# Performance work log

Measured on AMD Instinct MI355X. Metric: run time of the kernel, lower is better.

Reference implementation:

```python
import jax, jax.numpy as jnp
import numpy as np

IGNORE_INDEX = -100
BETA = 0.1
B, T, H, V = 4, 512, 4096, 32000

def setup_inputs() -> dict:
    key = jax.random.key(0)
    ks = jax.random.split(key, 8)
    s = 1.0 / np.sqrt(H)
    return {
        "_input": jax.random.normal(ks[0], (B, T, H), jnp.float32),
        "weight": jax.random.normal(ks[1], (V, H), jnp.float32) * s,
        "bias": jax.random.normal(ks[2], (V,), jnp.float32) * 0.01,
        "target": jax.random.randint(ks[3], (B, T), 0, V, jnp.int64),
        "preference_labels": jax.random.bernoulli(ks[4], 0.5, (B,)),
        "ref_input": jax.random.normal(ks[5], (B, T, H), jnp.float32),
        "ref_weight": jax.random.normal(ks[6], (V, H), jnp.float32) * s,
        "ref_bias": jax.random.normal(ks[7], (V,), jnp.float32) * 0.01,
        "kl": jax.random.uniform(jax.random.fold_in(key, 9), (1,), jnp.float32),
    }

def _avg_log_prob(x, w, b, target):
    # logits: [B, T, V]
    logits = jnp.einsum("bth,vh->btv", x, w) + b
    lse = jax.nn.logsumexp(logits, axis=-1)            # [B, T]
    idx = jnp.clip(target, 0, None)[..., None]
    tgt_logit = jnp.take_along_axis(logits, idx, axis=-1)[..., 0]
    per_tok_logp = tgt_logit - lse                     # [B, T]
    mask = (target != IGNORE_INDEX).astype(per_tok_logp.dtype)
    denom = jnp.maximum(mask.sum(-1), 1.0)
    return (per_tok_logp * mask).sum(-1) / denom       # [B]

def reference(_input, weight, bias, target, preference_labels, ref_input, ref_weight, ref_bias, kl):
    avg_logp = _avg_log_prob(_input, weight, bias, target)
    ref_avg_logp = jax.lax.stop_gradient(_avg_log_prob(ref_input, ref_weight, ref_bias, target))
    logratios = avg_logp - ref_avg_logp                # [B]
    multiplier = jnp.where(preference_labels, 1.0, -1.0)
    losses = 1.0 - jax.nn.sigmoid(BETA * (logratios - kl[0]) * multiplier)
    return losses.sum() / target.shape[0]
```

## Files before the change

kernel.cpp:

```cpp
#include <hip/hip_runtime.h>
#include <hip/hip_bf16.h>
#include <stdint.h>

#define HD 4096
#define VD 32000
#define BT 2048
#define TT 512
#define IGNORE_IDX (-100)

#define BM 256
#define BN 256
#define BKT 64
#define KT (HD / BKT)
#define NB (VD / BN)
#define MB (BT / BM)
#define NWG2 (MB * NB * 2)

#define NCHUNK (VD / 64)

typedef __attribute__((ext_vector_type(8))) short short8;
typedef __attribute__((ext_vector_type(4))) float f32x4;

__device__ __forceinline__ uint16_t f2bf(float f) {
    uint32_t u = __float_as_uint(f);
    u += 0x7FFFu + ((u >> 16) & 1u);
    return (uint16_t)(u >> 16);
}

__device__ __forceinline__ void gload16(const void* g, void* l) {
    __builtin_amdgcn_global_load_lds(
        (const __attribute__((address_space(1))) void*)g,
        (__attribute__((address_space(3))) void*)l, 16, 0, 0);
}

__global__ void convert_x(const float* __restrict__ x0, const float* __restrict__ x1,
                          uint16_t* __restrict__ xbf) {
    const int64_t n4 = (int64_t)BT * HD / 4;
    ushort4* o0 = (ushort4*)xbf;
    ushort4* o1 = (ushort4*)(xbf + (int64_t)BT * HD);
    for (int64_t i = blockIdx.x * (int64_t)blockDim.x + threadIdx.x; i < n4;
         i += (int64_t)gridDim.x * blockDim.x) {
        float4 a = ((const float4*)x0)[i];
        float4 b = ((const float4*)x1)[i];
        ushort4 ua, ub;
        ua.x = f2bf(a.x); ua.y = f2bf(a.y); ua.z = f2bf(a.z); ua.w = f2bf(a.w);
        ub.x = f2bf(b.x); ub.y = f2bf(b.y); ub.z = f2bf(b.z); ub.w = f2bf(b.w);
        o0[i] = ua;
        o1[i] = ub;
    }
}

__global__ void convert_w(const float* __restrict__ w0, const float* __restrict__ w1,
                          uint16_t* __restrict__ wbf) {
    const int64_t n4 = (int64_t)VD * HD / 4;
    ushort4* o0 = (ushort4*)wbf;
    ushort4* o1 = (ushort4*)(wbf + (int64_t)VD * HD);
    for (int64_t i = blockIdx.x * (int64_t)blockDim.x + threadIdx.x; i < n4;
         i += (int64_t)gridDim.x * blockDim.x) {
        float4 a = ((const float4*)w0)[i];
        float4 b = ((const float4*)w1)[i];
        ushort4 ua, ub;
        ua.x = f2bf(a.x); ua.y = f2bf(a.y); ua.z = f2bf(a.z); ua.w = f2bf(a.w);
        ub.x = f2bf(b.x); ub.y = f2bf(b.y); ub.z = f2bf(b.z); ub.w = f2bf(b.w);
        o0[i] = ua;
        o1[i] = ub;
    }
}

template<int CUR>
__device__ __forceinline__ void tile_body(
    int t,
    const uint16_t* __restrict__ agp, const uint16_t* __restrict__ bgp, int wid,
    const char* pA0, const char* pA1, const char* pB0, const char* pB1,
    uint16_t* As, uint16_t* Bs, f32x4 (&acc)[8][4])
{
    const int nxt = CUR ^ 1;
    const bool more = (t + 1) < KT;
    const int ko = (t + 1) * BKT;

    __builtin_amdgcn_sched_barrier(0);
    asm volatile("s_waitcnt vmcnt(4)" ::: "memory");
    __builtin_amdgcn_sched_barrier(0);
    __builtin_amdgcn_s_barrier();
    __builtin_amdgcn_sched_barrier(0);
    if (more) {
#pragma unroll
        for (int i = 0; i < 4; ++i)
            gload16(bgp + (size_t)i * 8 * HD + ko,
                    (char*)Bs + nxt * 32768 + wid * 4096 + i * 1024);
    }
    __builtin_amdgcn_sched_barrier(0);
    if (more) { asm volatile("s_waitcnt vmcnt(4)" ::: "memory"); }
    else      { asm volatile("s_waitcnt vmcnt(0)" ::: "memory"); }
    __builtin_amdgcn_sched_barrier(0);
    __builtin_amdgcn_s_barrier();
    __builtin_amdgcn_sched_barrier(0);
    if (more) {
#pragma unroll
        for (int i = 0; i < 4; ++i)
            gload16(agp + (size_t)i * 8 * HD + ko,
                    (char*)As + nxt * 32768 + wid * 4096 + i * 1024);
    }

#pragma unroll
    for (int ks = 0; ks < 2; ++ks) {
        const char* pA = ks ? pA1 : pA0;
        const char* pB = ks ? pB1 : pB0;
        short8 af[8], bf[4];
#pragma unroll
        for (int mi = 0; mi < 8; ++mi)
            af[mi] = *(const short8*)(pA + mi * 2048 + CUR * 32768);
#pragma unroll
        for (int ni = 0; ni < 4; ++ni)
            bf[ni] = *(const short8*)(pB + ni * 2048 + CUR * 32768);
        __builtin_amdgcn_s_setprio(1);
#pragma unroll
        for (int mi = 0; mi < 8; ++mi)
#pragma unroll
            for (int ni = 0; ni < 4; ++ni)
                acc[mi][ni] = __builtin_amdgcn_mfma_f32_16x16x32_bf16(
                    af[mi], bf[ni], acc[mi][ni], 0, 0, 0);
        __builtin_amdgcn_s_setprio(0);
    }
}

__global__ __launch_bounds__(512, 2) void gemm_lse_bf(
    const uint16_t* __restrict__ xbf, const uint16_t* __restrict__ wbf,
    const float* __restrict__ b0, const float* __restrict__ b1,
    const int* __restrict__ target,
    float* __restrict__ partials, float* __restrict__ tgtlog)
{
    __shared__ uint16_t As[2 * BM * BKT];
    __shared__ uint16_t Bs[2 * BN * BKT];

    const int orig = blockIdx.x;
    const int wgid = (orig & 7) * (NWG2 / 8) + (orig >> 3);
    const int mb    = wgid & 7;
    const int rest  = wgid >> 3;
    const int nb    = rest % NB;
    const int model = rest / NB;

    const uint16_t* xb = xbf + (size_t)model * BT * HD;
    const uint16_t* wb = wbf + (size_t)model * VD * HD;
    const float* bias  = model ? b1 : b0;

    const int row0 = mb * BM;
    const int c0   = nb * BN;

    const int tid    = threadIdx.x;
    const int lane   = tid & 63;
    const int wid    = tid >> 6;
    const int wr     = wid >> 2;
    const int wc     = wid & 3;

    const int lane15 = lane & 15;
    const int kg     = lane >> 4;
    const int swz    = (lane & 7) << 4;

    const int srow8 = lane >> 3;
    const int slot  = (lane & 7) ^ srow8;
    const uint16_t* agp = xb + (size_t)(row0 + wid * 32 + srow8) * HD + slot * 8;
    const uint16_t* bgp = wb + (size_t)(c0   + wid * 32 + srow8) * HD + slot * 8;

    const int arow_b = wr * 128 + lane15;
    const int brow_b = wc * 64 + lane15;
    const char* pA0 = (const char*)As + ((arow_b * 128 + 0  + kg * 16) ^ swz);
    const char* pA1 = (const char*)As + ((arow_b * 128 + 64 + kg * 16) ^ swz);
    const char* pB0 = (const char*)Bs + ((brow_b * 128 + 0  + kg * 16) ^ swz);
    const char* pB1 = (const char*)Bs + ((brow_b * 128 + 64 + kg * 16) ^ swz);

    f32x4 acc[8][4];
#pragma unroll
    for (int i = 0; i < 8; ++i)
#pragma unroll
        for (int j = 0; j < 4; ++j) acc[i][j] = (f32x4){0.f, 0.f, 0.f, 0.f};

#pragma unroll
    for (int i = 0; i < 4; ++i)
        gload16(bgp + (size_t)i * 8 * HD, (char*)Bs + wid * 4096 + i * 1024);
#pragma unroll
    for (int i = 0; i < 4; ++i)
        gload16(agp + (size_t)i * 8 * HD, (char*)As + wid * 4096 + i * 1024);

    for (int t2 = 0; t2 < KT; t2 += 2) {
        tile_body<0>(t2,     agp, bgp, wid, pA0, pA1, pB0, pB1, As, Bs, acc);
        tile_body<1>(t2 + 1, agp, bgp, wid, pA0, pA1, pB0, pB1, As, Bs, acc);
    }

    float bv4[4];
#pragma unroll
    for (int ni = 0; ni < 4; ++ni) bv4[ni] = bias[c0 + wc * 64 + ni * 16 + lane15];

#pragma unroll
    for (int mi = 0; mi < 8; ++mi) {
        const int grow_base = row0 + wr * 128 + mi * 16 + kg * 4;
#pragma unroll
        for (int j = 0; j < 4; ++j) {
            const int grow = grow_base + j;
            float v[4];
#pragma unroll
            for (int ni = 0; ni < 4; ++ni) v[ni] = acc[mi][ni][j] + bv4[ni];
            float m = fmaxf(fmaxf(v[0], v[1]), fmaxf(v[2], v[3]));
#pragma unroll
            for (int msk = 1; msk < 16; msk <<= 1)
                m = fmaxf(m, __shfl_xor(m, msk));
            float s = __expf(v[0] - m) + __expf(v[1] - m) +
                      __expf(v[2] - m) + __expf(v[3] - m);
#pragma unroll
            for (int msk = 1; msk < 16; msk <<= 1)
                s += __shfl_xor(s, msk);
            const int tg = target[grow];
#pragma unroll
            for (int ni = 0; ni < 4; ++ni) {
                const int gcol = c0 + wc * 64 + ni * 16 + lane15;
                if (tg == gcol) tgtlog[model * BT + grow] = v[ni];
            }
            if (lane15 == 0) {
                const size_t po = ((size_t)(model * BT + grow) * NCHUNK + nb * 4 + wc) * 2;
                partials[po]     = m;
                partials[po + 1] = s;
            }
        }
    }
}

__global__ __launch_bounds__(256) void gemm_lse_f32(
    const uint16_t* __restrict__ xbf,
    const float* __restrict__ w0, const float* __restrict__ b0,
    const float* __restrict__ w1, const float* __restrict__ b1,
    const int* __restrict__ target,
    float* __restrict__ partials, float* __restrict__ tgtlog)
{
    const int orig = blockIdx.x;
    const int wgid = (orig & 7) * 1000 + (orig >> 3);
    const int mb    = wgid & 7;
    const int rest  = wgid >> 3;
    const int chunk = rest % 500;
    const int model = rest / 500;

    const float* w    = model ? w1 : w0;
    const float* bias = model ? b1 : b0;
    const uint16_t* xb = xbf + (size_t)model * BT * HD;

    const int row0 = mb * 256;
    const int c0   = chunk * 64;

    const int tid  = threadIdx.x;
    const int lane = tid & 63;
    const int wid  = tid >> 6;

    __shared__ uint16_t As_[256 * 64];
    __shared__ uint16_t Bs_[64 * 64];

    f32x4 acc[4][4];
#pragma unroll
    for (int i = 0; i < 4; ++i)
#pragma unroll
        for (int j = 0; j < 4; ++j) acc[i][j] = (f32x4){0.f, 0.f, 0.f, 0.f};

    const int srow8 = lane >> 3;
    const int slot  = (lane & 7) ^ srow8;
    const uint16_t* agsrc = xb + (size_t)(row0 + wid * 64 + srow8) * HD + slot * 8;
    char* aldst = (char*)As_ + wid * 8192;

    const int ss   = tid & 7;
    const int srow = tid >> 3;
    const int swz_w = (srow & 7) << 4;
    const float* bptr = w + (size_t)(c0 + srow) * HD + ss * 8;

    const int lane15 = lane & 15;
    const int kg     = lane >> 4;
    const int swz_r  = (lane & 7) << 4;

    for (int kt = 0; kt < 64; ++kt) {
        const int kofs = kt * 64;
#pragma unroll
        for (int c = 0; c < 8; ++c)
            gload16(agsrc + (size_t)c * 8 * HD + kofs, aldst + c * 1024);
        {
            float4 bv[2][2];
#pragma unroll
            for (int r = 0; r < 2; ++r) {
                const float* p = bptr + (size_t)r * 32 * HD + kofs;
                bv[r][0] = *(const float4*)(p);
                bv[r][1] = *(const float4*)(p + 4);
            }
#pragma unroll
            for (int r = 0; r < 2; ++r) {
                const int row_l = srow + r * 32;
                float fv[8] = {bv[r][0].x, bv[r][0].y, bv[r][0].z, bv[r][0].w,
                               bv[r][1].x, bv[r][1].y, bv[r][1].z, bv[r][1].w};
                uint32_t pk[4];
#pragma unroll
                for (int e = 0; e < 4; ++e)
                    pk[e] = (uint32_t)f2bf(fv[2 * e]) | ((uint32_t)f2bf(fv[2 * e + 1]) << 16);
                const int off = (row_l * 128 + ss * 16) ^ swz_w;
                *(uint4*)((char*)Bs_ + off) = *(uint4*)pk;
            }
        }
        __syncthreads();
#pragma unroll
        for (int ks = 0; ks < 2; ++ks) {
            short8 af[4], bf[4];
#pragma unroll
            for (int mi = 0; mi < 4; ++mi) {
                const int arow = wid * 64 + mi * 16 + lane15;
                const int off = (arow * 128 + ks * 64 + kg * 16) ^ swz_r;
                af[mi] = *(const short8*)((const char*)As_ + off);
            }
#pragma unroll
            for (int ni = 0; ni < 4; ++ni) {
                const int brow = ni * 16 + lane15;
                const int off = (brow * 128 + ks * 64 + kg * 16) ^ swz_r;
                bf[ni] = *(const short8*)((const char*)Bs_ + off);
            }
#pragma unroll
            for (int mi = 0; mi < 4; ++mi)
#pragma unroll
                for (int ni = 0; ni < 4; ++ni)
                    acc[mi][ni] = __builtin_amdgcn_mfma_f32_16x16x32_bf16(
                        af[mi], bf[ni], acc[mi][ni], 0, 0, 0);
        }
        __syncthreads();
    }

    float bv4[4];
#pragma unroll
    for (int ni = 0; ni < 4; ++ni) bv4[ni] = bias[c0 + ni * 16 + lane15];

#pragma unroll
    for (int mi = 0; mi < 4; ++mi) {
        const int grow_base = row0 + wid * 64 + mi * 16 + kg * 4;
#pragma unroll
        for (int j = 0; j < 4; ++j) {
            const int grow = grow_base + j;
            float v[4];
#pragma unroll
            for (int ni = 0; ni < 4; ++ni) v[ni] = acc[mi][ni][j] + bv4[ni];
            float m = fmaxf(fmaxf(v[0], v[1]), fmaxf(v[2], v[3]));
#pragma unroll
            for (int msk = 1; msk < 16; msk <<= 1)
                m = fmaxf(m, __shfl_xor(m, msk));
            float s = __expf(v[0] - m) + __expf(v[1] - m) +
                      __expf(v[2] - m) + __expf(v[3] - m);
#pragma unroll
            for (int msk = 1; msk < 16; msk <<= 1)
                s += __shfl_xor(s, msk);
            const int tg = target[grow];
#pragma unroll
            for (int ni = 0; ni < 4; ++ni) {
                const int gcol = c0 + ni * 16 + lane15;
                if (tg == gcol) tgtlog[model * BT + grow] = v[ni];
            }
            if (lane15 == 0) {
                const size_t po = ((size_t)(model * BT + grow) * NCHUNK + chunk) * 2;
                partials[po]     = m;
                partials[po + 1] = s;
            }
        }
    }
}

__global__ void lse_reduce(const float* __restrict__ partials,
                           const float* __restrict__ tgtlog,
                           float* __restrict__ logp) {
    const int gw = blockIdx.x * (blockDim.x >> 6) + (threadIdx.x >> 6);
    if (gw >= 2 * BT) return;
    const int lane = threadIdx.x & 63;
    const float* p = partials + (size_t)gw * NCHUNK * 2;

    float m = -1e30f;
#pragma unroll
    for (int i = 0; i < 8; ++i) {
        const int c = lane + i * 64;
        if (c < NCHUNK) m = fmaxf(m, p[c * 2]);
    }
#pragma unroll
    for (int msk = 1; msk < 64; msk <<= 1) m = fmaxf(m, __shfl_xor(m, msk));
    float s = 0.f;
#pragma unroll
    for (int i = 0; i < 8; ++i) {
        const int c = lane + i * 64;
        if (c < NCHUNK) s += p[c * 2 + 1] * __expf(p[c * 2] - m);
    }
#pragma unroll
    for (int msk = 1; msk < 64; msk <<= 1) s += __shfl_xor(s, msk);
    if (lane == 0) {
        const float lse = m + __logf(s);
        logp[gw] = tgtlog[gw] - lse;
    }
}

__global__ void final_loss(const float* __restrict__ logp, const int* __restrict__ target,
                           const int* __restrict__ pref, const float* __restrict__ kl,
                           float* __restrict__ out) {
    const int t = threadIdx.x;
    const int lane = t & 63, wv = t >> 6;
    __shared__ float rp[4][8], rr[4][8], rm[4][8];
#pragma unroll
    for (int b = 0; b < 4; ++b) {
        const int idx = b * TT + t;
        const int tg = target[idx];
        const bool mk = (tg != IGNORE_IDX);
        float lp = mk ? logp[idx] : 0.f;
        float lr = mk ? logp[BT + idx] : 0.f;
        float mc = mk ? 1.f : 0.f;
        for (int off = 32; off; off >>= 1) {
            lp += __shfl_down(lp, off);
            lr += __shfl_down(lr, off);
            mc += __shfl_down(mc, off);
        }
        if (lane == 0) { rp[b][wv] = lp; rr[b][wv] = lr; rm[b][wv] = mc; }
    }
    __syncthreads();
    if (t == 0) {
        float loss = 0.f;
        for (int b = 0; b < 4; ++b) {
            float sp = 0.f, sr = 0.f, sm = 0.f;
            for (int i = 0; i < 8; ++i) { sp += rp[b][i]; sr += rr[b][i]; sm += rm[b][i]; }
            const float denom = fmaxf(sm, 1.f);
            const float lrb = (sp - sr) / denom;
            const float mult = pref[b] ? 1.f : -1.f;
            const float z = 0.1f * (lrb - kl[0]) * mult;
            loss += 1.f / (1.f + __expf(z));
        }
        out[0] = loss * 0.25f;
    }
}

extern "C" void kernel_launch(void* const* d_in, const int* in_sizes, int n_in,
                              void* d_out, int out_size, void* d_ws, size_t ws_size,
                              hipStream_t stream) {
    const float* x    = (const float*)d_in[0];
    const float* w0   = (const float*)d_in[1];
    const float* b0   = (const float*)d_in[2];
    const int*   tgt  = (const int*)d_in[3];
    const int*   pref = (const int*)d_in[4];
    const float* xr   = (const float*)d_in[5];
    const float* w1   = (const float*)d_in[6];
    const float* b1   = (const float*)d_in[7];
    const float* kl   = (const float*)d_in[8];
    float* out = (float*)d_out;

    const size_t xbf_b  = (size_t)2 * BT * HD * 2;
    const size_t part_b = (size_t)2 * BT * NCHUNK * 2 * 4;
    const size_t tl_b   = (size_t)2 * BT * 4;
    const size_t wbf_b  = (size_t)2 * VD * HD * 2;

    char* wp = (char*)d_ws;
    uint16_t* xbf     = (uint16_t*)wp;                 wp += xbf_b;
    float*    partials = (float*)wp;                   wp += part_b;
    float*    tgtlog   = (float*)wp;                   wp += tl_b;
    float*    logp     = (float*)wp;                   wp += tl_b;
    uint16_t* wbf      = (uint16_t*)wp;
    const bool use_wbf = ws_size >= (xbf_b + part_b + 2 * tl_b + wbf_b);

    hipLaunchKernelGGL(convert_x, dim3(1024), dim3(256), 0, stream, x, xr, xbf);
    if (use_wbf) {
        hipLaunchKernelGGL(convert_w, dim3(4096), dim3(256), 0, stream, w0, w1, wbf);
        hipLaunchKernelGGL(gemm_lse_bf, dim3(NWG2), dim3(512), 0, stream,
                           xbf, wbf, b0, b1, tgt, partials, tgtlog);
    } else {
        hipLaunchKernelGGL(gemm_lse_f32, dim3(8000), dim3(256), 0, stream,
                           xbf, w0, b0, w1, b1, tgt, partials, tgtlog);
    }
    hipLaunchKernelGGL(lse_reduce, dim3(2 * BT / 4), dim3(256), 0, stream,
                       partials, tgtlog, logp);
    hipLaunchKernelGGL(final_loss, dim3(1), dim3(512), 0, stream, logp, tgt, pref, kl, out);
}
```

Baseline: 1.543 ms.

## Interleave LDS fragment loads, global prefetch and MFMA in four phased sub-steps

Restructures the GEMM K-loop body into four phases. Each phase loads two A fragments and issues part of the next tile's global-to-LDS prefetch, then runs 16 MFMAs, with barriers between phases. The global-load row assignment is remapped so the rows each wave prefetches match the sub-phase that consumes them. The aim is to overlap LDS reads, async global loads and MFMA work more finely and to lower register pressure from holding all eight A fragments at once. The cost is many more workgroup barriers per tile, which may stall waves.

Result: faster. 1.291 ms (-16.3%).

```diff
diff --git a/kernel.cpp b/kernel.cpp
--- a/kernel.cpp
+++ b/kernel.cpp
@@ -32,6 +32,8 @@
         (const __attribute__((address_space(1))) void*)g,
         (__attribute__((address_space(3))) void*)l, 16, 0, 0);
 }
+
+#define SBAR __builtin_amdgcn_sched_barrier(0)
 
 __global__ void convert_x(const float* __restrict__ x0, const float* __restrict__ x1,
                           uint16_t* __restrict__ xbf) {
@@ -67,61 +69,96 @@
     }
 }
 
+__device__ __forceinline__ void mfma16(
+    const short8& a0k0, const short8& a0k1, const short8& a1k0, const short8& a1k1,
+    const short8 (&bfr)[4][2], f32x4* acc0, f32x4* acc1)
+{
+    __builtin_amdgcn_s_setprio(1);
+#pragma unroll
+    for (int ni = 0; ni < 4; ++ni)
+        acc0[ni] = __builtin_amdgcn_mfma_f32_16x16x32_bf16(a0k0, bfr[ni][0], acc0[ni], 0, 0, 0);
+#pragma unroll
+    for (int ni = 0; ni < 4; ++ni)
+        acc1[ni] = __builtin_amdgcn_mfma_f32_16x16x32_bf16(a1k0, bfr[ni][0], acc1[ni], 0, 0, 0);
+#pragma unroll
+    for (int ni = 0; ni < 4; ++ni)
+        acc0[ni] = __builtin_amdgcn_mfma_f32_16x16x32_bf16(a0k1, bfr[ni][1], acc0[ni], 0, 0, 0);
+#pragma unroll
+    for (int ni = 0; ni < 4; ++ni)
+        acc1[ni] = __builtin_amdgcn_mfma_f32_16x16x32_bf16(a1k1, bfr[ni][1], acc1[ni], 0, 0, 0);
+    __builtin_amdgcn_s_setprio(0);
+}
+
 template<int CUR>
 __device__ __forceinline__ void tile_body(
     int t,
-    const uint16_t* __restrict__ agp, const uint16_t* __restrict__ bgp, int wid,
+    const uint16_t* __restrict__ agp, const uint16_t* __restrict__ bgp,
+    char* aLdst, char* bLdst,
     const char* pA0, const char* pA1, const char* pB0, const char* pB1,
-    uint16_t* As, uint16_t* Bs, f32x4 (&acc)[8][4])
+    f32x4 (&acc)[8][4])
 {
-    const int nxt = CUR ^ 1;
+    constexpr int CB  = CUR * 32768;
+    constexpr int NXB = (CUR ^ 1) * 32768;
     const bool more = (t + 1) < KT;
     const int ko = (t + 1) * BKT;
 
-    __builtin_amdgcn_sched_barrier(0);
-    asm volatile("s_waitcnt vmcnt(4)" ::: "memory");
-    __builtin_amdgcn_sched_barrier(0);
-    __builtin_amdgcn_s_barrier();
-    __builtin_amdgcn_sched_barrier(0);
+    short8 bfr[4][2];
+    short8 af0k0, af0k1, af1k0, af1k1;
+
+#define BARR do { SBAR; __builtin_amdgcn_s_barrier(); SBAR; } while (0)
+#define LOAD_AF(mi0)                                                   \
+    af0k0 = *(const short8*)(pA0 + (mi0) * 2048 + CB);                 \
+    af0k1 = *(const short8*)(pA1 + (mi0) * 2048 + CB);                 \
+    af1k0 = *(const short8*)(pA0 + ((mi0) + 1) * 2048 + CB);           \
+    af1k1 = *(const short8*)(pA1 + ((mi0) + 1) * 2048 + CB);
+
+#pragma unroll
+    for (int ni = 0; ni < 4; ++ni) {
+        bfr[ni][0] = *(const short8*)(pB0 + ni * 2048 + CB);
+        bfr[ni][1] = *(const short8*)(pB1 + ni * 2048 + CB);
+    }
+    LOAD_AF(0);
     if (more) {
-#pragma unroll
-        for (int i = 0; i < 4; ++i)
-            gload16(bgp + (size_t)i * 8 * HD + ko,
-                    (char*)Bs + nxt * 32768 + wid * 4096 + i * 1024);
-    }
-    __builtin_amdgcn_sched_barrier(0);
-    if (more) { asm volatile("s_waitcnt vmcnt(4)" ::: "memory"); }
+        gload16(bgp + (size_t)(0 * 32) * HD + ko, bLdst + NXB + 0 * 4096);
+        gload16(bgp + (size_t)(1 * 32) * HD + ko, bLdst + NXB + 1 * 4096);
+    }
+    BARR;
+    mfma16(af0k0, af0k1, af1k0, af1k1, bfr, acc[0], acc[1]);
+    BARR;
+
+    LOAD_AF(2);
+    if (more) {
+        gload16(bgp + (size_t)(2 * 32) * HD + ko, bLdst + NXB + 2 * 4096);
+        gload16(bgp + (size_t)(3 * 32) * HD + ko, bLdst + NXB + 3 * 4096);
+    }
+    BARR;
+    mfma16(af0k0, af0k1, af1k0, af1k1, bfr, acc[2], acc[3]);
+    SBAR; asm volatile("s_waitcnt vmcnt(4)" ::: "memory"); SBAR;
+    BARR;
+
+    LOAD_AF(4);
+    if (more) {
+        gload16(agp + (size_t)(0 * 32) * HD + ko, aLdst + NXB + 0 * 4096);
+        gload16(agp + (size_t)(1 * 32) * HD + ko, aLdst + NXB + 1 * 4096);
+    }
+    BARR;
+    mfma16(af0k0, af0k1, af1k0, af1k1, bfr, acc[4], acc[5]);
+    BARR;
+
+    LOAD_AF(6);
+    if (more) {
+        gload16(agp + (size_t)(2 * 32) * HD + ko, aLdst + NXB + 2 * 4096);
+        gload16(agp + (size_t)(3 * 32) * HD + ko, aLdst + NXB + 3 * 4096);
+    }
+    BARR;
+    mfma16(af0k0, af0k1, af1k0, af1k1, bfr, acc[6], acc[7]);
+    SBAR;
+    if (more) { asm volatile("s_waitcnt vmcnt(2)" ::: "memory"); }
     else      { asm volatile("s_waitcnt vmcnt(0)" ::: "memory"); }
-    __builtin_amdgcn_sched_barrier(0);
-    __builtin_amdgcn_s_barrier();
-    __builtin_amdgcn_sched_barrier(0);
-    if (more) {
-#pragma unroll
-        for (int i = 0; i < 4; ++i)
-            gload16(agp + (size_t)i * 8 * HD + ko,
-                    (char*)As + nxt * 32768 + wid * 4096 + i * 1024);
-    }
-
-#pragma unroll
-    for (int ks = 0; ks < 2; ++ks) {
-        const char* pA = ks ? pA1 : pA0;
-        const char* pB = ks ? pB1 : pB0;
-        short8 af[8], bf[4];
-#pragma unroll
-        for (int mi = 0; mi < 8; ++mi)
-            af[mi] = *(const short8*)(pA + mi * 2048 + CUR * 32768);
-#pragma unroll
-        for (int ni = 0; ni < 4; ++ni)
-            bf[ni] = *(const short8*)(pB + ni * 2048 + CUR * 32768);
-        __builtin_amdgcn_s_setprio(1);
-#pragma unroll
-        for (int mi = 0; mi < 8; ++mi)
-#pragma unroll
-            for (int ni = 0; ni < 4; ++ni)
-                acc[mi][ni] = __builtin_amdgcn_mfma_f32_16x16x32_bf16(
-                    af[mi], bf[ni], acc[mi][ni], 0, 0, 0);
-        __builtin_amdgcn_s_setprio(0);
-    }
+    SBAR;
+    BARR;
+#undef LOAD_AF
+#undef BARR
 }
 
 __global__ __launch_bounds__(512, 2) void gemm_lse_bf(
@@ -159,8 +196,11 @@
 
     const int srow8 = lane >> 3;
     const int slot  = (lane & 7) ^ srow8;
-    const uint16_t* agp = xb + (size_t)(row0 + wid * 32 + srow8) * HD + slot * 8;
-    const uint16_t* bgp = wb + (size_t)(c0   + wid * 32 + srow8) * HD + slot * 8;
+    const uint16_t* agp = xb + (size_t)(row0 + wr * 128 + wc * 8 + srow8) * HD + slot * 8;
+    const int bq = wr * 2 + (wc & 1);
+    const uint16_t* bgp = wb + (size_t)(c0 + (wc >> 1) * 128 + bq * 8 + srow8) * HD + slot * 8;
+    char* aLdst = (char*)As + wr * 16384 + wc * 1024;
+    char* bLdst = (char*)Bs + (wc >> 1) * 16384 + bq * 1024;
 
     const int arow_b = wr * 128 + lane15;
     const int brow_b = wc * 64 + lane15;
@@ -176,15 +216,18 @@
         for (int j = 0; j < 4; ++j) acc[i][j] = (f32x4){0.f, 0.f, 0.f, 0.f};
 
 #pragma unroll
-    for (int i = 0; i < 4; ++i)
-        gload16(bgp + (size_t)i * 8 * HD, (char*)Bs + wid * 4096 + i * 1024);
-#pragma unroll
-    for (int i = 0; i < 4; ++i)
-        gload16(agp + (size_t)i * 8 * HD, (char*)As + wid * 4096 + i * 1024);
+    for (int j = 0; j < 4; ++j)
+        gload16(bgp + (size_t)(j * 32) * HD, bLdst + j * 4096);
+#pragma unroll
+    for (int j = 0; j < 4; ++j)
+        gload16(agp + (size_t)(j * 32) * HD, aLdst + j * 4096);
+    SBAR; asm volatile("s_waitcnt vmcnt(0)" ::: "memory"); SBAR;
+    __builtin_amdgcn_s_barrier();
+    SBAR;
 
     for (int t2 = 0; t2 < KT; t2 += 2) {
-        tile_body<0>(t2,     agp, bgp, wid, pA0, pA1, pB0, pB1, As, Bs, acc);
-        tile_body<1>(t2 + 1, agp, bgp, wid, pA0, pA1, pB0, pB1, As, Bs, acc);
+        tile_body<0>(t2,     agp, bgp, aLdst, bLdst, pA0, pA1, pB0, pB1, acc);
+        tile_body<1>(t2 + 1, agp, bgp, aLdst, bLdst, pA0, pA1, pB0, pB1, acc);
     }
 
     float bv4[4];
```

## Shrink bf16 GEMM tiles to 256x128x32 and simplify the LDS pipeline for occupancy

Applied to the files above, without the earlier changes.

Shrinks the bf16 GEMM-logsumexp tile from 256x256 with K-step 64 to 256x128 with K-step 32. The wave layout changes from 2x4 to 4x2, each wave holds a 4x4 accumulator block instead of 8x4, and the LDS swizzle is redone for the narrower tile. The split prefetch/barrier schedule is replaced by a simpler one: issue the next tile's loads, do the MFMAs, then wait for all loads and barrier once. Launch bounds rise to 4 workgroups per CU to hide latency with more concurrency, at the cost of less data reuse per tile, twice as many K iterations each with a full vmcnt(0) stall, and more partial LSE chunks written.

Result: faster. 1.458 ms (-5.5%).

```diff
diff --git a/kernel.cpp b/kernel.cpp
--- a/kernel.cpp
+++ b/kernel.cpp
@@ -9,8 +9,8 @@
 #define IGNORE_IDX (-100)
 
 #define BM 256
-#define BN 256
-#define BKT 64
+#define BN 128
+#define BKT 32
 #define KT (HD / BKT)
 #define NB (VD / BN)
 #define MB (BT / BM)
@@ -70,61 +70,43 @@
 template<int CUR>
 __device__ __forceinline__ void tile_body(
     int t,
-    const uint16_t* __restrict__ agp, const uint16_t* __restrict__ bgp, int wid,
-    const char* pA0, const char* pA1, const char* pB0, const char* pB1,
-    uint16_t* As, uint16_t* Bs, f32x4 (&acc)[8][4])
+    const uint16_t* __restrict__ agp, const uint16_t* __restrict__ bgp,
+    char* aLdst, char* bLdst,
+    const char* pA, const char* pB,
+    f32x4 (&acc)[4][4])
 {
-    const int nxt = CUR ^ 1;
+    constexpr int CA  = CUR * 16384;
+    constexpr int CBf = CUR * 8192;
+    constexpr int NXA = (CUR ^ 1) * 16384;
+    constexpr int NXB = (CUR ^ 1) * 8192;
     const bool more = (t + 1) < KT;
     const int ko = (t + 1) * BKT;
 
-    __builtin_amdgcn_sched_barrier(0);
-    asm volatile("s_waitcnt vmcnt(4)" ::: "memory");
-    __builtin_amdgcn_sched_barrier(0);
+    if (more) {
+        gload16(bgp + ko, bLdst + NXB);
+        gload16(agp + ko, aLdst + NXA);
+        gload16(agp + (size_t)16 * HD + ko, aLdst + NXA + 1024);
+    }
+
+    short8 bf[4], af[4];
+#pragma unroll
+    for (int ni = 0; ni < 4; ++ni)
+        bf[ni] = *(const short8*)(pB + ni * 1024 + CBf);
+#pragma unroll
+    for (int mi = 0; mi < 4; ++mi)
+        af[mi] = *(const short8*)(pA + mi * 1024 + CA);
+#pragma unroll
+    for (int mi = 0; mi < 4; ++mi)
+#pragma unroll
+        for (int ni = 0; ni < 4; ++ni)
+            acc[mi][ni] = __builtin_amdgcn_mfma_f32_16x16x32_bf16(
+                af[mi], bf[ni], acc[mi][ni], 0, 0, 0);
+
+    asm volatile("s_waitcnt vmcnt(0)" ::: "memory");
     __builtin_amdgcn_s_barrier();
-    __builtin_amdgcn_sched_barrier(0);
-    if (more) {
-#pragma unroll
-        for (int i = 0; i < 4; ++i)
-            gload16(bgp + (size_t)i * 8 * HD + ko,
-                    (char*)Bs + nxt * 32768 + wid * 4096 + i * 1024);
-    }
-    __builtin_amdgcn_sched_barrier(0);
-    if (more) { asm volatile("s_waitcnt vmcnt(4)" ::: "memory"); }
-    else      { asm volatile("s_waitcnt vmcnt(0)" ::: "memory"); }
-    __builtin_amdgcn_sched_barrier(0);
-    __builtin_amdgcn_s_barrier();
-    __builtin_amdgcn_sched_barrier(0);
-    if (more) {
-#pragma unroll
-        for (int i = 0; i < 4; ++i)
-            gload16(agp + (size_t)i * 8 * HD + ko,
-                    (char*)As + nxt * 32768 + wid * 4096 + i * 1024);
-    }
-
-#pragma unroll
-    for (int ks = 0; ks < 2; ++ks) {
-        const char* pA = ks ? pA1 : pA0;
-        const char* pB = ks ? pB1 : pB0;
-        short8 af[8], bf[4];
-#pragma unroll
-        for (int mi = 0; mi < 8; ++mi)
-            af[mi] = *(const short8*)(pA + mi * 2048 + CUR * 32768);
-#pragma unroll
-        for (int ni = 0; ni < 4; ++ni)
-            bf[ni] = *(const short8*)(pB + ni * 2048 + CUR * 32768);
-        __builtin_amdgcn_s_setprio(1);
-#pragma unroll
-        for (int mi = 0; mi < 8; ++mi)
-#pragma unroll
-            for (int ni = 0; ni < 4; ++ni)
-                acc[mi][ni] = __builtin_amdgcn_mfma_f32_16x16x32_bf16(
-                    af[mi], bf[ni], acc[mi][ni], 0, 0, 0);
-        __builtin_amdgcn_s_setprio(0);
-    }
-}
-
-__global__ __launch_bounds__(512, 2) void gemm_lse_bf(
+}
+
+__global__ __launch_bounds__(512, 4) void gemm_lse_bf(
     const uint16_t* __restrict__ xbf, const uint16_t* __restrict__ wbf,
     const float* __restrict__ b0, const float* __restrict__ b1,
     const int* __restrict__ target,
@@ -150,41 +132,38 @@
     const int tid    = threadIdx.x;
     const int lane   = tid & 63;
     const int wid    = tid >> 6;
-    const int wr     = wid >> 2;
-    const int wc     = wid & 3;
+    const int wr     = wid >> 1;
+    const int wc     = wid & 1;
 
     const int lane15 = lane & 15;
     const int kg     = lane >> 4;
-    const int swz    = (lane & 7) << 4;
-
-    const int srow8 = lane >> 3;
-    const int slot  = (lane & 7) ^ srow8;
-    const uint16_t* agp = xb + (size_t)(row0 + wid * 32 + srow8) * HD + slot * 8;
-    const uint16_t* bgp = wb + (size_t)(c0   + wid * 32 + srow8) * HD + slot * 8;
-
-    const int arow_b = wr * 128 + lane15;
-    const int brow_b = wc * 64 + lane15;
-    const char* pA0 = (const char*)As + ((arow_b * 128 + 0  + kg * 16) ^ swz);
-    const char* pA1 = (const char*)As + ((arow_b * 128 + 64 + kg * 16) ^ swz);
-    const char* pB0 = (const char*)Bs + ((brow_b * 128 + 0  + kg * 16) ^ swz);
-    const char* pB1 = (const char*)Bs + ((brow_b * 128 + 64 + kg * 16) ^ swz);
-
-    f32x4 acc[8][4];
-#pragma unroll
-    for (int i = 0; i < 8; ++i)
+
+    const int srow  = lane >> 2;
+    const int gslot = (lane & 3) ^ ((lane >> 3) & 3);
+    const uint16_t* agp = xb + (size_t)(row0 + wid * 32 + srow) * HD + gslot * 8;
+    const uint16_t* bgp = wb + (size_t)(c0 + wid * 16 + srow) * HD + gslot * 8;
+    char* aLdst = (char*)As + wid * 2048;
+    char* bLdst = (char*)Bs + wid * 1024;
+
+    const int rswz = ((kg ^ ((lane15 >> 1) & 3)) << 4);
+    const char* pA = (const char*)As + (wr * 64 + lane15) * 64 + rswz;
+    const char* pB = (const char*)Bs + (wc * 64 + lane15) * 64 + rswz;
+
+    f32x4 acc[4][4];
+#pragma unroll
+    for (int i = 0; i < 4; ++i)
 #pragma unroll
         for (int j = 0; j < 4; ++j) acc[i][j] = (f32x4){0.f, 0.f, 0.f, 0.f};
 
-#pragma unroll
-    for (int i = 0; i < 4; ++i)
-        gload16(bgp + (size_t)i * 8 * HD, (char*)Bs + wid * 4096 + i * 1024);
-#pragma unroll
-    for (int i = 0; i < 4; ++i)
-        gload16(agp + (size_t)i * 8 * HD, (char*)As + wid * 4096 + i * 1024);
+    gload16(bgp, bLdst);
+    gload16(agp, aLdst);
+    gload16(agp + (size_t)16 * HD, aLdst + 1024);
+    asm volatile("s_waitcnt vmcnt(0)" ::: "memory");
+    __builtin_amdgcn_s_barrier();
 
     for (int t2 = 0; t2 < KT; t2 += 2) {
-        tile_body<0>(t2,     agp, bgp, wid, pA0, pA1, pB0, pB1, As, Bs, acc);
-        tile_body<1>(t2 + 1, agp, bgp, wid, pA0, pA1, pB0, pB1, As, Bs, acc);
+        tile_body<0>(t2,     agp, bgp, aLdst, bLdst, pA, pB, acc);
+        tile_body<1>(t2 + 1, agp, bgp, aLdst, bLdst, pA, pB, acc);
     }
 
     float bv4[4];
@@ -192,8 +171,8 @@
     for (int ni = 0; ni < 4; ++ni) bv4[ni] = bias[c0 + wc * 64 + ni * 16 + lane15];
 
 #pragma unroll
-    for (int mi = 0; mi < 8; ++mi) {
-        const int grow_base = row0 + wr * 128 + mi * 16 + kg * 4;
+    for (int mi = 0; mi < 4; ++mi) {
+        const int grow_base = row0 + wr * 64 + mi * 16 + kg * 4;
 #pragma unroll
         for (int j = 0; j < 4; ++j) {
             const int grow = grow_base + j;
@@ -216,7 +195,7 @@
                 if (tg == gcol) tgtlog[model * BT + grow] = v[ni];
             }
             if (lane15 == 0) {
-                const size_t po = ((size_t)(model * BT + grow) * NCHUNK + nb * 4 + wc) * 2;
+                const size_t po = ((size_t)(model * BT + grow) * NCHUNK + nb * 2 + wc) * 2;
                 partials[po]     = m;
                 partials[po + 1] = s;
             }
```
